# Performance work log

Hardware: AMD Instinct MI355X
Metric: run time of the kernel (lower is better)

The kernel has to match this reference:

```python
import jax, jax.numpy as jnp
import numpy as np

N_HEAD = 4
D_MODEL = 256
FEAT_DIM = 256
D_K = D_MODEL // N_HEAD  # 64
TEMP = float(np.sqrt(D_K))
LN_EPS = 1e-5


def setup_inputs() -> dict:
    key = jax.random.key(0)
    ks = jax.random.split(key, 12)
    B, N_src, N_ngh = 2048, 1, 128
    src = jax.random.normal(ks[0], (B, N_src, FEAT_DIM), dtype=jnp.float32)
    seq = jax.random.normal(ks[1], (B, N_ngh, FEAT_DIM), dtype=jnp.float32)
    mask = jax.random.randint(ks[2], (B, N_ngh), 0, 2) > 0
    s_qk = np.sqrt(2.0 / (D_MODEL + D_K))
    w_qs = jax.random.normal(ks[3], (N_HEAD * D_K, D_MODEL), dtype=jnp.float32) * s_qk
    w_ks = jax.random.normal(ks[4], (N_HEAD * D_K, D_MODEL), dtype=jnp.float32) * s_qk
    w_vs = jax.random.normal(ks[5], (N_HEAD * D_K, D_MODEL), dtype=jnp.float32) * s_qk
    fc_w = jax.random.normal(ks[6], (D_MODEL, N_HEAD * D_K), dtype=jnp.float32) * 0.05
    fc_b = jnp.zeros((D_MODEL,), dtype=jnp.float32)
    ln_g = jnp.ones((D_MODEL,), dtype=jnp.float32)
    ln_b = jnp.zeros((D_MODEL,), dtype=jnp.float32)
    fc1_w = jax.random.normal(ks[7], (FEAT_DIM, 2 * D_MODEL), dtype=jnp.float32) * 0.05
    fc1_b = jnp.zeros((FEAT_DIM,), dtype=jnp.float32)
    fc2_w = jax.random.normal(ks[8], (FEAT_DIM, FEAT_DIM), dtype=jnp.float32) * 0.05
    fc2_b = jnp.zeros((FEAT_DIM,), dtype=jnp.float32)
    return {"src": src, "seq": seq, "mask": mask, "w_qs": w_qs, "w_ks": w_ks,
            "w_vs": w_vs, "fc_w": fc_w, "fc_b": fc_b, "ln_g": ln_g, "ln_b": ln_b,
            "fc1_w": fc1_w, "fc1_b": fc1_b, "fc2_w": fc2_w, "fc2_b": fc2_b}


def _forward(src, seq, mask, w_qs, w_ks, w_vs, fc_w, fc_b, ln_g, ln_b,
             fc1_w, fc1_b, fc2_w, fc2_b):
    B, N_src, _ = src.shape
    N_ngh = seq.shape[1]
    nn_ = N_ngh // N_src
    # projections (dropout is identity in eval mode)
    qh = (src @ w_qs.T).reshape(B, N_src, N_HEAD, D_K)              # bshd
    kh = (seq @ w_ks.T).reshape(B, N_src, nn_, N_HEAD, D_K)        # bsnhd
    vh = (seq @ w_vs.T).reshape(B, N_src, nn_, N_HEAD, D_K)
    scores = jnp.einsum('bshd,bsnhd->bshn', qh, kh) / TEMP          # [B,Ns,H,nn]
    # Replicate original mask layout exactly: attn rows are flat in (b,s,h)
    # order, but mask was built with .repeat(n_head,1,1) -> head-major tiling.
    flat = scores.reshape(B * N_src * N_HEAD, nn_)
    mask_rep = jnp.tile(mask.reshape(B * N_src, nn_), (N_HEAD, 1))  # [H*B*Ns, nn]
    flat = jnp.where(mask_rep, -1e10, flat)
    attn = jax.nn.softmax(flat, axis=-1).reshape(B, N_src, N_HEAD, nn_)
    out = jnp.einsum('bshn,bsnhd->bshd', attn, vh).reshape(B, N_src, N_HEAD * D_K)
    out = out @ fc_w.T + fc_b
    x = out + src  # residual (q == src since pos_dim == 0)
    mu = jnp.mean(x, axis=-1, keepdims=True)
    var = jnp.mean(jnp.square(x - mu), axis=-1, keepdims=True)
    x = (x - mu) * jax.lax.rsqrt(var + LN_EPS) * ln_g + ln_b
    # MergeLayer (non_linear=True)
    h = jax.nn.relu(jnp.concatenate([x, src], axis=-1) @ fc1_w.T + fc1_b)
    z = h @ fc2_w.T + fc2_b                                        # [B,Ns,feat]
    return z, attn


def reference(src, seq, mask, w_qs, w_ks, w_vs, fc_w, fc_b, ln_g, ln_b,
              fc1_w, fc1_b, fc2_w, fc2_b):
    return _forward(src, seq, mask, w_qs, w_ks, w_vs, fc_w, fc_b, ln_g, ln_b,
                    fc1_w, fc1_b, fc2_w, fc2_b)
```

## Files before the change

kernel.cpp:

```cpp
#include <hip/hip_runtime.h>

typedef unsigned int uint32;
typedef unsigned short ushort16;

#define DI __device__ __forceinline__

#define BATCH 2048
#define NN    128
#define DM    256
#define NH    4
#define DK    64

DI float bf2f(ushort16 h) { return __uint_as_float(((uint32)h) << 16); }

DI ushort16 f2bf(float f) {
    uint32 u = __float_as_uint(f);
    uint32 r = u + 0x7fffu + ((u >> 16) & 1u);
    return (ushort16)(r >> 16);
}

DI void unpack8(const uint4 v, float f[8]) {
    f[0] = __uint_as_float(v.x << 16);
    f[1] = __uint_as_float(v.x & 0xffff0000u);
    f[2] = __uint_as_float(v.y << 16);
    f[3] = __uint_as_float(v.y & 0xffff0000u);
    f[4] = __uint_as_float(v.z << 16);
    f[5] = __uint_as_float(v.z & 0xffff0000u);
    f[6] = __uint_as_float(v.w << 16);
    f[7] = __uint_as_float(v.w & 0xffff0000u);
}

DI float dot8(const float* a, const float f[8], float acc) {
    acc = fmaf(a[0], f[0], acc);
    acc = fmaf(a[1], f[1], acc);
    acc = fmaf(a[2], f[2], acc);
    acc = fmaf(a[3], f[3], acc);
    acc = fmaf(a[4], f[4], acc);
    acc = fmaf(a[5], f[5], acc);
    acc = fmaf(a[6], f[6], acc);
    acc = fmaf(a[7], f[7], acc);
    return acc;
}

#define WOFF_QS  0
#define WOFF_KS  65536
#define WOFF_VS  131072
#define WOFF_FC  196608
#define WOFF_FC1 262144
#define WOFF_FC2 393216

__global__ __launch_bounds__(256) void prep_kernel(
    const float* __restrict__ wqs, const float* __restrict__ wks,
    const float* __restrict__ wvs, const float* __restrict__ fcw,
    const float* __restrict__ fc1w, const float* __restrict__ fc2w,
    ushort16* __restrict__ out)
{
    const int bid = blockIdx.x;
    const float* srcp; size_t soff, doff;
    if (bid < 64)       { srcp = wqs;  soff = (size_t)bid * 1024;         doff = WOFF_QS;  }
    else if (bid < 128) { srcp = wks;  soff = (size_t)(bid - 64) * 1024;  doff = WOFF_KS;  }
    else if (bid < 192) { srcp = wvs;  soff = (size_t)(bid - 128) * 1024; doff = WOFF_VS;  }
    else if (bid < 256) { srcp = fcw;  soff = (size_t)(bid - 192) * 1024; doff = WOFF_FC;  }
    else if (bid < 384) { srcp = fc1w; soff = (size_t)(bid - 256) * 1024; doff = WOFF_FC1; }
    else                { srcp = fc2w; soff = (size_t)(bid - 384) * 1024; doff = WOFF_FC2; }
    const int t = threadIdx.x;
    float4 v = *(const float4*)(srcp + soff + t * 4);
    uint2 pk;
    pk.x = (uint32)f2bf(v.x) | ((uint32)f2bf(v.y) << 16);
    pk.y = (uint32)f2bf(v.z) | ((uint32)f2bf(v.w) << 16);
    *(uint2*)(out + doff + soff + t * 4) = pk;
}

__global__ __launch_bounds__(256) void qu_kernel(
    const float* __restrict__ src, const ushort16* __restrict__ wbf,
    float* __restrict__ u)
{
    __shared__ float sS[8][DM];
    __shared__ float sQ[8][DM];
    const int t  = threadIdx.x;
    const int b0 = blockIdx.x * 8;

    #pragma unroll
    for (int r = 0; r < 8; ++r) sS[r][t] = src[(size_t)(b0 + r) * DM + t];
    __syncthreads();

    {
        float acc[8] = {0.f,0.f,0.f,0.f,0.f,0.f,0.f,0.f};
        const ushort16* wrow = wbf + WOFF_QS + (size_t)t * DM;
        for (int kc = 0; kc < DM; kc += 8) {
            uint4 w8 = *(const uint4*)(wrow + kc);
            float wf[8]; unpack8(w8, wf);
            #pragma unroll
            for (int r = 0; r < 8; ++r) acc[r] = dot8(&sS[r][kc], wf, acc[r]);
        }
        #pragma unroll
        for (int r = 0; r < 8; ++r) sQ[r][t] = acc[r];
    }
    __syncthreads();

    const ushort16* wks = wbf + WOFF_KS;
    for (int h = 0; h < NH; ++h) {
        float ua[8] = {0.f,0.f,0.f,0.f,0.f,0.f,0.f,0.f};
        for (int dc = 0; dc < DK; dc += 8) {
            float wv[8];
            #pragma unroll
            for (int e = 0; e < 8; ++e)
                wv[e] = bf2f(wks[(size_t)(h * DK + dc + e) * DM + t]);
            #pragma unroll
            for (int r = 0; r < 8; ++r) {
                float4 qa = *(const float4*)&sQ[r][h * DK + dc];
                float4 qb = *(const float4*)&sQ[r][h * DK + dc + 4];
                float a = ua[r];
                a = fmaf(qa.x, wv[0], a); a = fmaf(qa.y, wv[1], a);
                a = fmaf(qa.z, wv[2], a); a = fmaf(qa.w, wv[3], a);
                a = fmaf(qb.x, wv[4], a); a = fmaf(qb.y, wv[5], a);
                a = fmaf(qb.z, wv[6], a); a = fmaf(qb.w, wv[7], a);
                ua[r] = a;
            }
        }
        #pragma unroll
        for (int r = 0; r < 8; ++r)
            u[(size_t)(b0 + r) * (NH * DM) + h * DM + t] = ua[r] * 0.125f;
    }
}

#define SEQ_STRIDE 264
#define U_STRIDE   264

__global__ __launch_bounds__(256) void attn_kernel(
    const float* __restrict__ seq, const int* __restrict__ mask,
    const float* __restrict__ u, float* __restrict__ c,
    float* __restrict__ attn_out)
{
    __shared__ ushort16 sseq[NN * SEQ_STRIDE];
    __shared__ float    sbuf[2048];
    __shared__ float    sattn[NN * NH];

    const int t = threadIdx.x;
    const int b = blockIdx.x;

    #pragma unroll
    for (int i = 0; i < 4; ++i)
        sbuf[i * U_STRIDE + t] = u[(size_t)b * 1024 + i * 256 + t];

    const float* sp = seq + (size_t)b * (NN * DM);
    #pragma unroll
    for (int it = 0; it < 32; ++it) {
        int idx = it * 1024 + t * 4;
        int row = idx >> 8, col = idx & 255;
        float4 v = *(const float4*)(sp + idx);
        uint2 pk;
        pk.x = (uint32)f2bf(v.x) | ((uint32)f2bf(v.y) << 16);
        pk.y = (uint32)f2bf(v.z) | ((uint32)f2bf(v.w) << 16);
        *(uint2*)&sseq[row * SEQ_STRIDE + col] = pk;
    }
    __syncthreads();

    {
        const int h  = t & 3;
        const int n0 = t >> 2;
        const float* uh = &sbuf[h * U_STRIDE];
        const ushort16* r0 = &sseq[n0 * SEQ_STRIDE];
        const ushort16* r1 = &sseq[(n0 + 64) * SEQ_STRIDE];
        float s0 = 0.f, s1 = 0.f;
        for (int kc = 0; kc < DM; kc += 8) {
            uint4 va = *(const uint4*)(r0 + kc);
            uint4 vb = *(const uint4*)(r1 + kc);
            float fa[8], fb[8];
            unpack8(va, fa); unpack8(vb, fb);
            s0 = dot8(&uh[kc], fa, s0);
            s1 = dot8(&uh[kc], fb, s1);
        }
        int mr = (4 * b + h) & (BATCH - 1);
        if (mask[(size_t)mr * NN + n0] != 0)      s0 = -1e10f;
        if (mask[(size_t)mr * NN + n0 + 64] != 0) s1 = -1e10f;
        sattn[n0 * 4 + h]        = s0;
        sattn[(n0 + 64) * 4 + h] = s1;
    }
    __syncthreads();

    {
        const int w = t >> 6, l = t & 63;
        float x0 = sattn[l * 4 + w], x1 = sattn[(l + 64) * 4 + w];
        float mx = fmaxf(x0, x1);
        #pragma unroll
        for (int o = 32; o > 0; o >>= 1) mx = fmaxf(mx, __shfl_xor(mx, o, 64));
        float e0 = __expf(x0 - mx), e1 = __expf(x1 - mx);
        float sm = e0 + e1;
        #pragma unroll
        for (int o = 32; o > 0; o >>= 1) sm += __shfl_xor(sm, o, 64);
        float inv = 1.f / sm;
        float a0 = e0 * inv, a1 = e1 * inv;
        sattn[l * 4 + w]        = a0;
        sattn[(l + 64) * 4 + w] = a1;
        attn_out[(size_t)b * (NH * NN) + w * NN + l]      = a0;
        attn_out[(size_t)b * (NH * NN) + w * NN + l + 64] = a1;
    }
    __syncthreads();

    {
        const int ng = t >> 7;
        const int jp = t & 127;
        float cc[4][2] = {{0.f,0.f},{0.f,0.f},{0.f,0.f},{0.f,0.f}};
        for (int i = 0; i < 64; ++i) {
            int n = ng * 64 + i;
            uint32 v = *(const uint32*)&sseq[n * SEQ_STRIDE + jp * 2];
            float f0 = __uint_as_float(v << 16);
            float f1 = __uint_as_float(v & 0xffff0000u);
            float4 at = *(const float4*)&sattn[n * 4];
            cc[0][0] = fmaf(at.x, f0, cc[0][0]); cc[0][1] = fmaf(at.x, f1, cc[0][1]);
            cc[1][0] = fmaf(at.y, f0, cc[1][0]); cc[1][1] = fmaf(at.y, f1, cc[1][1]);
            cc[2][0] = fmaf(at.z, f0, cc[2][0]); cc[2][1] = fmaf(at.z, f1, cc[2][1]);
            cc[3][0] = fmaf(at.w, f0, cc[3][0]); cc[3][1] = fmaf(at.w, f1, cc[3][1]);
        }
        __syncthreads();
        #pragma unroll
        for (int h = 0; h < 4; ++h) {
            sbuf[ng * 1024 + h * 256 + jp * 2]     = cc[h][0];
            sbuf[ng * 1024 + h * 256 + jp * 2 + 1] = cc[h][1];
        }
    }
    __syncthreads();
    #pragma unroll
    for (int h = 0; h < 4; ++h)
        c[(size_t)b * 1024 + h * 256 + t] = sbuf[h * 256 + t] + sbuf[1024 + h * 256 + t];
}

__global__ __launch_bounds__(256) void mlp_kernel(
    const float* __restrict__ c, const float* __restrict__ src,
    const ushort16* __restrict__ wbf,
    const float* __restrict__ fcb, const float* __restrict__ lng,
    const float* __restrict__ lnb, const float* __restrict__ fc1b,
    const float* __restrict__ fc2b, float* __restrict__ zout)
{
    __shared__ float sC[8][1024];
    __shared__ float sA[8][256];
    __shared__ float sX[8][256];
    __shared__ float sS[8][256];
    __shared__ float sH[8][256];
    __shared__ float sRed[4][8][2];

    const int t  = threadIdx.x;
    const int b0 = blockIdx.x * 8;
    const int h  = t >> 6;

    #pragma unroll
    for (int i = 0; i < 8; ++i)
        *(float4*)&sC[i][t * 4] = *(const float4*)&c[(size_t)(b0 + i) * 1024 + t * 4];
    #pragma unroll
    for (int r = 0; r < 8; ++r) sS[r][t] = src[(size_t)(b0 + r) * DM + t];
    __syncthreads();

    {
        float acc[8] = {0.f,0.f,0.f,0.f,0.f,0.f,0.f,0.f};
        const ushort16* wr = wbf + WOFF_VS + (size_t)t * DM;
        for (int kc = 0; kc < DM; kc += 8) {
            uint4 w8 = *(const uint4*)(wr + kc);
            float wf[8]; unpack8(w8, wf);
            #pragma unroll
            for (int r = 0; r < 8; ++r) acc[r] = dot8(&sC[r][h * 256 + kc], wf, acc[r]);
        }
        #pragma unroll
        for (int r = 0; r < 8; ++r) sA[r][t] = acc[r];
    }
    __syncthreads();

    float xv[8];
    {
        float acc[8] = {0.f,0.f,0.f,0.f,0.f,0.f,0.f,0.f};
        const ushort16* wr = wbf + WOFF_FC + (size_t)t * DM;
        for (int kc = 0; kc < DM; kc += 8) {
            uint4 w8 = *(const uint4*)(wr + kc);
            float wf[8]; unpack8(w8, wf);
            #pragma unroll
            for (int r = 0; r < 8; ++r) acc[r] = dot8(&sA[r][kc], wf, acc[r]);
        }
        float bb = fcb[t];
        #pragma unroll
        for (int r = 0; r < 8; ++r) xv[r] = acc[r] + bb + sS[r][t];
    }
    {
        const int w = t >> 6, l = t & 63;
        #pragma unroll
        for (int r = 0; r < 8; ++r) {
            float vs = xv[r], vq = xv[r] * xv[r];
            #pragma unroll
            for (int o = 32; o > 0; o >>= 1) {
                vs += __shfl_xor(vs, o, 64);
                vq += __shfl_xor(vq, o, 64);
            }
            if (l == 0) { sRed[w][r][0] = vs; sRed[w][r][1] = vq; }
        }
        __syncthreads();
        float g = lng[t], bb = lnb[t];
        #pragma unroll
        for (int r = 0; r < 8; ++r) {
            float S = sRed[0][r][0] + sRed[1][r][0] + sRed[2][r][0] + sRed[3][r][0];
            float Q = sRed[0][r][1] + sRed[1][r][1] + sRed[2][r][1] + sRed[3][r][1];
            float mu  = S * (1.f / 256.f);
            float var = Q * (1.f / 256.f) - mu * mu;
            float rs  = rsqrtf(var + 1e-5f);
            sX[r][t] = (xv[r] - mu) * rs * g + bb;
        }
    }
    __syncthreads();

    {
        float acc[8] = {0.f,0.f,0.f,0.f,0.f,0.f,0.f,0.f};
        const ushort16* wr = wbf + WOFF_FC1 + (size_t)t * 512;
        for (int kc = 0; kc < 256; kc += 8) {
            uint4 w8 = *(const uint4*)(wr + kc);
            float wf[8]; unpack8(w8, wf);
            #pragma unroll
            for (int r = 0; r < 8; ++r) acc[r] = dot8(&sX[r][kc], wf, acc[r]);
        }
        for (int kc = 0; kc < 256; kc += 8) {
            uint4 w8 = *(const uint4*)(wr + 256 + kc);
            float wf[8]; unpack8(w8, wf);
            #pragma unroll
            for (int r = 0; r < 8; ++r) acc[r] = dot8(&sS[r][kc], wf, acc[r]);
        }
        float bb = fc1b[t];
        #pragma unroll
        for (int r = 0; r < 8; ++r) sH[r][t] = fmaxf(acc[r] + bb, 0.f);
    }
    __syncthreads();

    {
        float acc[8] = {0.f,0.f,0.f,0.f,0.f,0.f,0.f,0.f};
        const ushort16* wr = wbf + WOFF_FC2 + (size_t)t * DM;
        for (int kc = 0; kc < DM; kc += 8) {
            uint4 w8 = *(const uint4*)(wr + kc);
            float wf[8]; unpack8(w8, wf);
            #pragma unroll
            for (int r = 0; r < 8; ++r) acc[r] = dot8(&sH[r][kc], wf, acc[r]);
        }
        float bb = fc2b[t];
        #pragma unroll
        for (int r = 0; r < 8; ++r)
            zout[(size_t)(b0 + r) * DM + t] = acc[r] + bb;
    }
}

extern "C" void kernel_launch(void* const* d_in, const int* in_sizes, int n_in,
                              void* d_out, int out_size, void* d_ws, size_t ws_size,
                              hipStream_t stream)
{
    const float* src  = (const float*)d_in[0];
    const float* seq  = (const float*)d_in[1];
    const int*   mask = (const int*)d_in[2];
    const float* wqs  = (const float*)d_in[3];
    const float* wks  = (const float*)d_in[4];
    const float* wvs  = (const float*)d_in[5];
    const float* fcw  = (const float*)d_in[6];
    const float* fcb  = (const float*)d_in[7];
    const float* lng  = (const float*)d_in[8];
    const float* lnb  = (const float*)d_in[9];
    const float* fc1w = (const float*)d_in[10];
    const float* fc1b = (const float*)d_in[11];
    const float* fc2w = (const float*)d_in[12];
    const float* fc2b = (const float*)d_in[13];

    float* zout     = (float*)d_out;
    float* attn_out = zout + (size_t)BATCH * DM;

    float* u = (float*)d_ws;
    float* cbuf = u + (size_t)BATCH * 1024;
    ushort16* wbf = (ushort16*)(cbuf + (size_t)BATCH * 1024);

    prep_kernel<<<448, 256, 0, stream>>>(wqs, wks, wvs, fcw, fc1w, fc2w, wbf);
    qu_kernel<<<256, 256, 0, stream>>>(src, wbf, u);
    attn_kernel<<<BATCH, 256, 0, stream>>>(seq, mask, u, cbuf, attn_out);
    mlp_kernel<<<256, 256, 0, stream>>>(cbuf, src, wbf, fcb, lng, lnb,
                                        fc1b, fc2b, zout);
}
```

Baseline: 472.2 us.

## Stream seq into LDS with direct global-to-LDS loads and split-softmax attention

The attention kernel now loads each batch's fp32 seq tile straight into LDS with global_load_lds, using an XOR swizzle, and skips the bf16 conversion pass. It runs 512 threads, each wave owning 16 neighbor rows and computing a partial softmax and weighted sum, then merges the per-wave partials through LDS with max/sum rescaling. The Wk weights are stored transposed so the qu kernel reads them with vector loads, and qu uses 4 rows per block across twice as many blocks. The fp32 LDS tile (128 KB) limits occupancy to one block per CU and doubles LDS traffic, in exchange for removing conversion work and an extra sync phase.

```diff
diff --git a/kernel.cpp b/kernel.cpp
--- a/kernel.cpp
+++ b/kernel.cpp
@@ -10,6 +10,11 @@
 #define DM    256
 #define NH    4
 #define DK    64
+
+#define GLOAD_LDS16(g, s) \
+  __builtin_amdgcn_global_load_lds( \
+      (const __attribute__((address_space(1))) unsigned int*)(g), \
+      (__attribute__((address_space(3))) unsigned int*)(s), 16, 0, 0)
 
 DI float bf2f(ushort16 h) { return __uint_as_float(((uint32)h) << 16); }
 
@@ -56,14 +61,23 @@
     ushort16* __restrict__ out)
 {
     const int bid = blockIdx.x;
+    const int t   = threadIdx.x;
+    if (bid >= 64 && bid < 128) {
+        int base = (bid - 64) * 1024 + t * 4;
+        float4 v = *(const float4*)(wks + base);
+        int r = base >> 8, c = base & 255;
+        out[WOFF_KS + (size_t)(c + 0) * 256 + r] = f2bf(v.x);
+        out[WOFF_KS + (size_t)(c + 1) * 256 + r] = f2bf(v.y);
+        out[WOFF_KS + (size_t)(c + 2) * 256 + r] = f2bf(v.z);
+        out[WOFF_KS + (size_t)(c + 3) * 256 + r] = f2bf(v.w);
+        return;
+    }
     const float* srcp; size_t soff, doff;
     if (bid < 64)       { srcp = wqs;  soff = (size_t)bid * 1024;         doff = WOFF_QS;  }
-    else if (bid < 128) { srcp = wks;  soff = (size_t)(bid - 64) * 1024;  doff = WOFF_KS;  }
     else if (bid < 192) { srcp = wvs;  soff = (size_t)(bid - 128) * 1024; doff = WOFF_VS;  }
     else if (bid < 256) { srcp = fcw;  soff = (size_t)(bid - 192) * 1024; doff = WOFF_FC;  }
     else if (bid < 384) { srcp = fc1w; soff = (size_t)(bid - 256) * 1024; doff = WOFF_FC1; }
     else                { srcp = fc2w; soff = (size_t)(bid - 384) * 1024; doff = WOFF_FC2; }
-    const int t = threadIdx.x;
     float4 v = *(const float4*)(srcp + soff + t * 4);
     uint2 pk;
     pk.x = (uint32)f2bf(v.x) | ((uint32)f2bf(v.y) << 16);
@@ -75,155 +89,171 @@
     const float* __restrict__ src, const ushort16* __restrict__ wbf,
     float* __restrict__ u)
 {
-    __shared__ float sS[8][DM];
-    __shared__ float sQ[8][DM];
+    __shared__ float sS[4][DM];
+    __shared__ float sQ[4][DM];
     const int t  = threadIdx.x;
-    const int b0 = blockIdx.x * 8;
-
-    #pragma unroll
-    for (int r = 0; r < 8; ++r) sS[r][t] = src[(size_t)(b0 + r) * DM + t];
-    __syncthreads();
-
-    {
-        float acc[8] = {0.f,0.f,0.f,0.f,0.f,0.f,0.f,0.f};
+    const int b0 = blockIdx.x * 4;
+
+    #pragma unroll
+    for (int r = 0; r < 4; ++r) sS[r][t] = src[(size_t)(b0 + r) * DM + t];
+    __syncthreads();
+
+    {
+        float acc[4] = {0.f,0.f,0.f,0.f};
         const ushort16* wrow = wbf + WOFF_QS + (size_t)t * DM;
+        #pragma unroll 2
         for (int kc = 0; kc < DM; kc += 8) {
             uint4 w8 = *(const uint4*)(wrow + kc);
             float wf[8]; unpack8(w8, wf);
             #pragma unroll
-            for (int r = 0; r < 8; ++r) acc[r] = dot8(&sS[r][kc], wf, acc[r]);
-        }
-        #pragma unroll
-        for (int r = 0; r < 8; ++r) sQ[r][t] = acc[r];
-    }
-    __syncthreads();
-
-    const ushort16* wks = wbf + WOFF_KS;
+            for (int r = 0; r < 4; ++r) acc[r] = dot8(&sS[r][kc], wf, acc[r]);
+        }
+        #pragma unroll
+        for (int r = 0; r < 4; ++r) sQ[r][t] = acc[r];
+    }
+    __syncthreads();
+
+    const ushort16* wr2 = wbf + WOFF_KS + (size_t)t * DM;
+    #pragma unroll
     for (int h = 0; h < NH; ++h) {
-        float ua[8] = {0.f,0.f,0.f,0.f,0.f,0.f,0.f,0.f};
+        float ua[4] = {0.f,0.f,0.f,0.f};
+        #pragma unroll 2
         for (int dc = 0; dc < DK; dc += 8) {
-            float wv[8];
-            #pragma unroll
-            for (int e = 0; e < 8; ++e)
-                wv[e] = bf2f(wks[(size_t)(h * DK + dc + e) * DM + t]);
-            #pragma unroll
-            for (int r = 0; r < 8; ++r) {
-                float4 qa = *(const float4*)&sQ[r][h * DK + dc];
-                float4 qb = *(const float4*)&sQ[r][h * DK + dc + 4];
-                float a = ua[r];
-                a = fmaf(qa.x, wv[0], a); a = fmaf(qa.y, wv[1], a);
-                a = fmaf(qa.z, wv[2], a); a = fmaf(qa.w, wv[3], a);
-                a = fmaf(qb.x, wv[4], a); a = fmaf(qb.y, wv[5], a);
-                a = fmaf(qb.z, wv[6], a); a = fmaf(qb.w, wv[7], a);
-                ua[r] = a;
-            }
-        }
-        #pragma unroll
-        for (int r = 0; r < 8; ++r)
+            uint4 w8 = *(const uint4*)(wr2 + h * DK + dc);
+            float wf[8]; unpack8(w8, wf);
+            #pragma unroll
+            for (int r = 0; r < 4; ++r) ua[r] = dot8(&sQ[r][h * DK + dc], wf, ua[r]);
+        }
+        #pragma unroll
+        for (int r = 0; r < 4; ++r)
             u[(size_t)(b0 + r) * (NH * DM) + h * DM + t] = ua[r] * 0.125f;
     }
 }
 
-#define SEQ_STRIDE 264
-#define U_STRIDE   264
-
-__global__ __launch_bounds__(256) void attn_kernel(
+#define USTRIDE 276
+
+__global__ __launch_bounds__(512) void attn_kernel(
     const float* __restrict__ seq, const int* __restrict__ mask,
     const float* __restrict__ u, float* __restrict__ c,
     float* __restrict__ attn_out)
 {
-    __shared__ ushort16 sseq[NN * SEQ_STRIDE];
-    __shared__ float    sbuf[2048];
-    __shared__ float    sattn[NN * NH];
+    __shared__ float sq[NN * DM];
+    __shared__ float sU[NH * USTRIDE];
+    __shared__ float sM[8][4];
+    __shared__ float sSg[8][4];
 
     const int t = threadIdx.x;
     const int b = blockIdx.x;
-
-    #pragma unroll
-    for (int i = 0; i < 4; ++i)
-        sbuf[i * U_STRIDE + t] = u[(size_t)b * 1024 + i * 256 + t];
+    const int w = t >> 6, l = t & 63;
+    const int ln = l >> 2, h = l & 3;
+
+    if (t < 256) {
+        float4 v = *(const float4*)(u + (size_t)b * 1024 + t * 4);
+        int hh = t >> 6, j = (t & 63) * 4;
+        *(float4*)&sU[hh * USTRIDE + j] = v;
+    }
+    __syncthreads();
 
     const float* sp = seq + (size_t)b * (NN * DM);
     #pragma unroll
-    for (int it = 0; it < 32; ++it) {
-        int idx = it * 1024 + t * 4;
-        int row = idx >> 8, col = idx & 255;
-        float4 v = *(const float4*)(sp + idx);
-        uint2 pk;
-        pk.x = (uint32)f2bf(v.x) | ((uint32)f2bf(v.y) << 16);
-        pk.y = (uint32)f2bf(v.z) | ((uint32)f2bf(v.w) << 16);
-        *(uint2*)&sseq[row * SEQ_STRIDE + col] = pk;
-    }
-    __syncthreads();
-
-    {
-        const int h  = t & 3;
-        const int n0 = t >> 2;
-        const float* uh = &sbuf[h * U_STRIDE];
-        const ushort16* r0 = &sseq[n0 * SEQ_STRIDE];
-        const ushort16* r1 = &sseq[(n0 + 64) * SEQ_STRIDE];
-        float s0 = 0.f, s1 = 0.f;
-        for (int kc = 0; kc < DM; kc += 8) {
-            uint4 va = *(const uint4*)(r0 + kc);
-            uint4 vb = *(const uint4*)(r1 + kc);
-            float fa[8], fb[8];
-            unpack8(va, fa); unpack8(vb, fb);
-            s0 = dot8(&uh[kc], fa, s0);
-            s1 = dot8(&uh[kc], fb, s1);
-        }
+    for (int i = 0; i < 16; ++i) {
+        const int r = w * 16 + i;
+        const float* ga = sp + r * DM + ((l ^ (r & 7)) << 2);
+        GLOAD_LDS16(ga, &sq[r * DM]);
+    }
+    asm volatile("s_waitcnt vmcnt(0)" ::: "memory");
+    __builtin_amdgcn_sched_barrier(0);
+
+    const int rr = w * 16 + ln;
+    float s = 0.f;
+    {
+        const float* urow = &sU[h * USTRIDE];
+        const int rsw = rr & 7;
+        #pragma unroll 8
+        for (int g = 0; g < 64; ++g) {
+            float4 sv = *(const float4*)&sq[rr * DM + ((g ^ rsw) << 2)];
+            float4 uv = *(const float4*)&urow[g * 4];
+            s = fmaf(uv.x, sv.x, s);
+            s = fmaf(uv.y, sv.y, s);
+            s = fmaf(uv.z, sv.z, s);
+            s = fmaf(uv.w, sv.w, s);
+        }
+    }
+    {
         int mr = (4 * b + h) & (BATCH - 1);
-        if (mask[(size_t)mr * NN + n0] != 0)      s0 = -1e10f;
-        if (mask[(size_t)mr * NN + n0 + 64] != 0) s1 = -1e10f;
-        sattn[n0 * 4 + h]        = s0;
-        sattn[(n0 + 64) * 4 + h] = s1;
-    }
-    __syncthreads();
-
-    {
-        const int w = t >> 6, l = t & 63;
-        float x0 = sattn[l * 4 + w], x1 = sattn[(l + 64) * 4 + w];
-        float mx = fmaxf(x0, x1);
-        #pragma unroll
-        for (int o = 32; o > 0; o >>= 1) mx = fmaxf(mx, __shfl_xor(mx, o, 64));
-        float e0 = __expf(x0 - mx), e1 = __expf(x1 - mx);
-        float sm = e0 + e1;
-        #pragma unroll
-        for (int o = 32; o > 0; o >>= 1) sm += __shfl_xor(sm, o, 64);
-        float inv = 1.f / sm;
-        float a0 = e0 * inv, a1 = e1 * inv;
-        sattn[l * 4 + w]        = a0;
-        sattn[(l + 64) * 4 + w] = a1;
-        attn_out[(size_t)b * (NH * NN) + w * NN + l]      = a0;
-        attn_out[(size_t)b * (NH * NN) + w * NN + l + 64] = a1;
-    }
-    __syncthreads();
-
-    {
-        const int ng = t >> 7;
-        const int jp = t & 127;
-        float cc[4][2] = {{0.f,0.f},{0.f,0.f},{0.f,0.f},{0.f,0.f}};
-        for (int i = 0; i < 64; ++i) {
-            int n = ng * 64 + i;
-            uint32 v = *(const uint32*)&sseq[n * SEQ_STRIDE + jp * 2];
-            float f0 = __uint_as_float(v << 16);
-            float f1 = __uint_as_float(v & 0xffff0000u);
-            float4 at = *(const float4*)&sattn[n * 4];
-            cc[0][0] = fmaf(at.x, f0, cc[0][0]); cc[0][1] = fmaf(at.x, f1, cc[0][1]);
-            cc[1][0] = fmaf(at.y, f0, cc[1][0]); cc[1][1] = fmaf(at.y, f1, cc[1][1]);
-            cc[2][0] = fmaf(at.z, f0, cc[2][0]); cc[2][1] = fmaf(at.z, f1, cc[2][1]);
-            cc[3][0] = fmaf(at.w, f0, cc[3][0]); cc[3][1] = fmaf(at.w, f1, cc[3][1]);
-        }
-        __syncthreads();
-        #pragma unroll
-        for (int h = 0; h < 4; ++h) {
-            sbuf[ng * 1024 + h * 256 + jp * 2]     = cc[h][0];
-            sbuf[ng * 1024 + h * 256 + jp * 2 + 1] = cc[h][1];
-        }
-    }
-    __syncthreads();
-    #pragma unroll
-    for (int h = 0; h < 4; ++h)
-        c[(size_t)b * 1024 + h * 256 + t] = sbuf[h * 256 + t] + sbuf[1024 + h * 256 + t];
+        if (mask[(size_t)mr * NN + rr] != 0) s = -1e10f;
+    }
+    float m = s;
+    m = fmaxf(m, __shfl_xor(m, 4));
+    m = fmaxf(m, __shfl_xor(m, 8));
+    m = fmaxf(m, __shfl_xor(m, 16));
+    m = fmaxf(m, __shfl_xor(m, 32));
+    float ev = __expf(s - m);
+    float sg = ev;
+    sg += __shfl_xor(sg, 4);
+    sg += __shfl_xor(sg, 8);
+    sg += __shfl_xor(sg, 16);
+    sg += __shfl_xor(sg, 32);
+
+    float cc[4][4];
+    #pragma unroll
+    for (int hh = 0; hh < 4; ++hh) {
+        cc[hh][0] = 0.f; cc[hh][1] = 0.f; cc[hh][2] = 0.f; cc[hh][3] = 0.f;
+    }
+    #pragma unroll
+    for (int i = 0; i < 16; ++i) {
+        float e0 = __shfl(ev, i * 4 + 0);
+        float e1 = __shfl(ev, i * 4 + 1);
+        float e2 = __shfl(ev, i * 4 + 2);
+        float e3 = __shfl(ev, i * 4 + 3);
+        const int r = w * 16 + i;
+        float4 sv = *(const float4*)&sq[r * DM + ((l ^ (r & 7)) << 2)];
+        cc[0][0] = fmaf(e0, sv.x, cc[0][0]); cc[0][1] = fmaf(e0, sv.y, cc[0][1]);
+        cc[0][2] = fmaf(e0, sv.z, cc[0][2]); cc[0][3] = fmaf(e0, sv.w, cc[0][3]);
+        cc[1][0] = fmaf(e1, sv.x, cc[1][0]); cc[1][1] = fmaf(e1, sv.y, cc[1][1]);
+        cc[1][2] = fmaf(e1, sv.z, cc[1][2]); cc[1][3] = fmaf(e1, sv.w, cc[1][3]);
+        cc[2][0] = fmaf(e2, sv.x, cc[2][0]); cc[2][1] = fmaf(e2, sv.y, cc[2][1]);
+        cc[2][2] = fmaf(e2, sv.z, cc[2][2]); cc[2][3] = fmaf(e2, sv.w, cc[2][3]);
+        cc[3][0] = fmaf(e3, sv.x, cc[3][0]); cc[3][1] = fmaf(e3, sv.y, cc[3][1]);
+        cc[3][2] = fmaf(e3, sv.z, cc[3][2]); cc[3][3] = fmaf(e3, sv.w, cc[3][3]);
+    }
+
+    #pragma unroll
+    for (int hh = 0; hh < 4; ++hh) {
+        #pragma unroll
+        for (int k = 0; k < 4; ++k)
+            sq[w * 4096 + hh * 256 + l * 4 + k] = cc[hh][k];
+    }
+    if (l < 4) { sM[w][l] = m; sSg[w][l] = sg; }
+    __syncthreads();
+
+    {
+        float M = sM[0][h];
+        #pragma unroll
+        for (int w2 = 1; w2 < 8; ++w2) M = fmaxf(M, sM[w2][h]);
+        float S = 0.f;
+        #pragma unroll
+        for (int w2 = 0; w2 < 8; ++w2) S += sSg[w2][h] * __expf(sM[w2][h] - M);
+        float p = ev * __expf(m - M) / S;
+        attn_out[(size_t)b * (NH * NN) + h * NN + rr] = p;
+    }
+
+    #pragma unroll
+    for (int rep = 0; rep < 2; ++rep) {
+        int idx = t + rep * 512;
+        int hh = idx >> 8, j = idx & 255;
+        float M = sM[0][hh];
+        #pragma unroll
+        for (int w2 = 1; w2 < 8; ++w2) M = fmaxf(M, sM[w2][hh]);
+        float S = 0.f, acc = 0.f;
+        #pragma unroll
+        for (int w2 = 0; w2 < 8; ++w2) {
+            float sc = __expf(sM[w2][hh] - M);
+            S   += sSg[w2][hh] * sc;
+            acc += sq[w2 * 4096 + hh * 256 + j] * sc;
+        }
+        c[(size_t)b * 1024 + idx] = acc / S;
+    }
 }
 
 __global__ __launch_bounds__(256) void mlp_kernel(
@@ -369,8 +399,8 @@
     ushort16* wbf = (ushort16*)(cbuf + (size_t)BATCH * 1024);
 
     prep_kernel<<<448, 256, 0, stream>>>(wqs, wks, wvs, fcw, fc1w, fc2w, wbf);
-    qu_kernel<<<256, 256, 0, stream>>>(src, wbf, u);
-    attn_kernel<<<BATCH, 256, 0, stream>>>(seq, mask, u, cbuf, attn_out);
+    qu_kernel<<<512, 256, 0, stream>>>(src, wbf, u);
+    attn_kernel<<<BATCH, 512, 0, stream>>>(seq, mask, u, cbuf, attn_out);
     mlp_kernel<<<256, 256, 0, stream>>>(cbuf, src, wbf, fcb, lng, lnb,
                                         fc1b, fc2b, zout);
 }
```

Result: no change. 465.6 us (-1.4%).
